# Kernel optimization log

Hardware: AMD Instinct MI355X
Metric: run time of the kernel (lower is better)

## Reference

```python
import jax, jax.numpy as jnp
import numpy as np

D_MODEL = 2048
N_HEADS = 16
HEAD_DIM = D_MODEL // N_HEADS


def setup_inputs() -> dict:
    key = jax.random.key(0)
    ks = jax.random.split(key, 9)
    s = 0.02
    B, S = 4, 2048
    return {
        "x": jax.random.normal(ks[0], (B, S, D_MODEL), dtype=jnp.float32),
        "Wq": jax.random.normal(ks[1], (D_MODEL, D_MODEL), dtype=jnp.float32) * s,
        "bq": jnp.zeros((D_MODEL,), dtype=jnp.float32),
        "Wk": jax.random.normal(ks[2], (D_MODEL, D_MODEL), dtype=jnp.float32) * s,
        "bk": jnp.zeros((D_MODEL,), dtype=jnp.float32),
        "Wv": jax.random.normal(ks[3], (D_MODEL, D_MODEL), dtype=jnp.float32) * s,
        "bv": jnp.zeros((D_MODEL,), dtype=jnp.float32),
        "Wo": jax.random.normal(ks[4], (D_MODEL, D_MODEL), dtype=jnp.float32) * s,
        "bo": jnp.zeros((D_MODEL,), dtype=jnp.float32),
    }


def reference(x, Wq, bq, Wk, bk, Wv, bv, Wo, bo):
    B, S, _ = x.shape
    scale = jnp.asarray(np.sqrt(HEAD_DIM), dtype=x.dtype)

    def split_heads(t):  # [B,S,D] -> [B,H,S,hd]
        return t.reshape(B, S, N_HEADS, HEAD_DIM).transpose(0, 2, 1, 3)

    q = split_heads(x @ Wq + bq)
    k = split_heads(x @ Wk + bk)
    v = split_heads(x @ Wv + bv)

    # scores: [B,H,S,S]
    attn = jnp.einsum('bhqd,bhkd->bhqk', q, k) / scale
    kv_len = S
    causal = jnp.triu(jnp.ones((S, kv_len), dtype=bool), k=kv_len - S + 1)
    attn = jnp.where(causal[None, None], -jnp.inf, attn)
    attn = jax.nn.softmax(attn, axis=-1)
    # dropout is identity (p=0 / eval mode)
    out = jnp.einsum('bhqk,bhkd->bhqd', attn, v)
    out = out.transpose(0, 2, 1, 3).reshape(B, S, D_MODEL)
    return out @ Wo + bo
```

## Files before the change

### kernel.cpp

```cpp
#include <hip/hip_runtime.h>
#include <hip/hip_bf16.h>

#define DEV __device__ __forceinline__

typedef __bf16 bf16_t;
typedef __bf16 bf16x8 __attribute__((ext_vector_type(8)));
typedef __bf16 bf16x4 __attribute__((ext_vector_type(4)));
typedef float f32x4 __attribute__((ext_vector_type(4)));
typedef float f32x16 __attribute__((ext_vector_type(16)));
typedef unsigned int u32;
typedef unsigned short u16;
typedef u32 u32x4 __attribute__((ext_vector_type(4)));

constexpr int D_MODEL = 2048;
constexpr int SEQ = 2048;
constexpr int BATCH = 4;
constexpr int N_HEADS = 16;
constexpr int HEAD_DIM = 128;
constexpr int TOK = BATCH * SEQ;

DEV void gload_lds16(const void* g, void* l) {
  __builtin_amdgcn_global_load_lds(
      (const __attribute__((address_space(1))) unsigned int*)g,
      (__attribute__((address_space(3))) unsigned int*)l, 16, 0, 0);
}

DEV float fast_exp2(float x) {
#if __has_builtin(__builtin_amdgcn_exp2f)
  return __builtin_amdgcn_exp2f(x);
#else
  return exp2f(x);
#endif
}

DEV u32 pack2(float lo, float hi) {
  u16 a = __builtin_bit_cast(u16, (bf16_t)lo);
  u16 b = __builtin_bit_cast(u16, (bf16_t)hi);
  return (u32)a | ((u32)b << 16);
}

#define MFMA16(a, b, c) __builtin_amdgcn_mfma_f32_16x16x32_bf16((a), (b), (c), 0, 0, 0)
#define MFMA32(a, b, c) __builtin_amdgcn_mfma_f32_32x32x16_bf16((a), (b), (c), 0, 0, 0)

__global__ void k_cvt(const float* __restrict__ in, bf16_t* __restrict__ out, int n4) {
  int i = blockIdx.x * blockDim.x + threadIdx.x;
  int stride = gridDim.x * blockDim.x;
  for (; i < n4; i += stride) {
    float4 v = ((const float4*)in)[i];
    bf16x4 o;
    o[0] = (bf16_t)v.x; o[1] = (bf16_t)v.y; o[2] = (bf16_t)v.z; o[3] = (bf16_t)v.w;
    ((bf16x4*)out)[i] = o;
  }
}

__global__ void k_transpose_w4(const float* __restrict__ Wq, const float* __restrict__ Wk,
                               const float* __restrict__ Wv, const float* __restrict__ Wo,
                               bf16_t* __restrict__ WqkvT, bf16_t* __restrict__ WoT) {
  __shared__ float t[32][33];
  const int z = blockIdx.z;
  const float* W = z == 0 ? Wq : z == 1 ? Wk : z == 2 ? Wv : Wo;
  bf16_t* Wt = z < 3 ? WqkvT + (size_t)z * D_MODEL * D_MODEL : WoT;
  int k0 = blockIdx.x * 32, n0 = blockIdx.y * 32;
  int tx = threadIdx.x, ty = threadIdx.y;
#pragma unroll
  for (int r = ty; r < 32; r += 8)
    t[r][tx] = W[(size_t)(k0 + r) * D_MODEL + n0 + tx];
  __syncthreads();
#pragma unroll
  for (int r = ty; r < 32; r += 8)
    Wt[(size_t)(n0 + r) * D_MODEL + k0 + tx] = (bf16_t)t[tx][r];
}

template <int MODE>
__global__ __launch_bounds__(512, 2) void k_gemm256(const bf16_t* __restrict__ A,
                                                    const bf16_t* __restrict__ Bt,
                                                    const float* __restrict__ b0p,
                                                    const float* __restrict__ b1p,
                                                    const float* __restrict__ b2p,
                                                    void* __restrict__ o0,
                                                    void* __restrict__ o1,
                                                    void* __restrict__ o2) {
  constexpr int K = D_MODEL;
  constexpr int NTOT = (MODE == 0) ? 3 * D_MODEL : D_MODEL;
  constexpr int NT = K / 64;
  __shared__ __attribute__((aligned(16))) bf16_t sh[2][2][2][8192];

  const int bid = blockIdx.x;
  const int nbn = NTOT / 256;
  const int cpx = gridDim.x >> 3;
  const int swz = (bid & 7) * cpx + (bid >> 3);
  const int bm = swz / nbn, bn = swz % nbn;

  const int tid = threadIdx.x;
  const int lane = tid & 63;
  const int w = tid >> 6;
  const int wm = w >> 2, wn = w & 3;
  const int lr = lane & 15, lg = lane >> 4;

  const bf16_t* Agl[2];
  const bf16_t* Bgl[2];
  int ldsg[2];
#pragma unroll
  for (int l = 0; l < 2; ++l) {
    int g = l * 512 + tid;
    int r = g >> 2, c = g & 3;
    int csw = c ^ ((r ^ (r >> 2)) & 3);
    Agl[l] = A + (size_t)(bm * 256 + r) * K + csw * 8;
    Bgl[l] = Bt + (size_t)(bn * 256 + r) * K + csw * 8;
    ldsg[l] = g * 8;
  }

  auto SA = [&](int buf, int t, int kh) {
    const int off = t * 64 + kh * 32;
#pragma unroll
    for (int l = 0; l < 2; ++l) gload_lds16(Agl[l] + off, &sh[buf][0][kh][ldsg[l]]);
  };
  auto SB = [&](int buf, int t, int kh) {
    const int off = t * 64 + kh * 32;
#pragma unroll
    for (int l = 0; l < 2; ++l) gload_lds16(Bgl[l] + off, &sh[buf][1][kh][ldsg[l]]);
  };

  int offA[8], offB[4];
  const int cx = lg ^ ((lr ^ (lr >> 2)) & 3);
#pragma unroll
  for (int i = 0; i < 8; ++i) offA[i] = (wm * 128 + i * 16 + lr) * 32 + cx * 8;
#pragma unroll
  for (int j = 0; j < 4; ++j) offB[j] = (wn * 64 + j * 16 + lr) * 32 + cx * 8;

  f32x4 acc[8][4] = {};
  bf16x8 a0[8], a1[8], bb[4];

  SA(0, 0, 0); SB(0, 0, 0); SA(0, 0, 1); SB(0, 0, 1); SA(1, 1, 0);

  for (int t = 0; t < NT; ++t) {
    const int cur = t & 1, nxt = cur ^ 1;
    const int t1 = (t + 1 < NT) ? t + 1 : NT - 1;
    const int t2 = (t + 2 < NT) ? t + 2 : NT - 1;

    asm volatile("s_waitcnt vmcnt(6)" ::: "memory");
    __builtin_amdgcn_s_barrier();
#pragma unroll
    for (int i = 0; i < 8; ++i) a0[i] = *(const bf16x8*)&sh[cur][0][0][offA[i]];
#pragma unroll
    for (int j = 0; j < 4; ++j) bb[j] = *(const bf16x8*)&sh[cur][1][0][offB[j]];
    SB(nxt, t1, 0);
    asm volatile("s_waitcnt lgkmcnt(0)" ::: "memory");
    __builtin_amdgcn_sched_barrier(0);
    __builtin_amdgcn_s_setprio(1);
#pragma unroll
    for (int i = 0; i < 8; ++i) {
      acc[i][0] = MFMA16(a0[i], bb[0], acc[i][0]);
      acc[i][1] = MFMA16(a0[i], bb[1], acc[i][1]);
    }
    __builtin_amdgcn_s_setprio(0);

    asm volatile("s_waitcnt vmcnt(6)" ::: "memory");
    __builtin_amdgcn_s_barrier();
#pragma unroll
    for (int i = 0; i < 8; ++i) a1[i] = *(const bf16x8*)&sh[cur][0][1][offA[i]];
    SA(nxt, t1, 1);
    asm volatile("s_waitcnt lgkmcnt(0)" ::: "memory");
    __builtin_amdgcn_sched_barrier(0);
    __builtin_amdgcn_s_setprio(1);
#pragma unroll
    for (int i = 0; i < 8; ++i) {
      acc[i][2] = MFMA16(a0[i], bb[2], acc[i][2]);
      acc[i][3] = MFMA16(a0[i], bb[3], acc[i][3]);
    }
    __builtin_amdgcn_s_setprio(0);

    asm volatile("s_waitcnt vmcnt(6)" ::: "memory");
    __builtin_amdgcn_s_barrier();
#pragma unroll
    for (int j = 0; j < 4; ++j) bb[j] = *(const bf16x8*)&sh[cur][1][1][offB[j]];
    SB(nxt, t1, 1);
    asm volatile("s_waitcnt lgkmcnt(0)" ::: "memory");
    __builtin_amdgcn_sched_barrier(0);
    __builtin_amdgcn_s_setprio(1);
#pragma unroll
    for (int i = 0; i < 8; ++i) {
      acc[i][0] = MFMA16(a1[i], bb[0], acc[i][0]);
      acc[i][1] = MFMA16(a1[i], bb[1], acc[i][1]);
    }
    __builtin_amdgcn_s_setprio(0);

    SA(cur, t2, 0);
    __builtin_amdgcn_s_setprio(1);
#pragma unroll
    for (int i = 0; i < 8; ++i) {
      acc[i][2] = MFMA16(a1[i], bb[2], acc[i][2]);
      acc[i][3] = MFMA16(a1[i], bb[3], acc[i][3]);
    }
    __builtin_amdgcn_s_setprio(0);
  }

#pragma unroll
  for (int i = 0; i < 8; ++i) {
    const int row = bm * 256 + wm * 128 + i * 16 + lg * 4;
#pragma unroll
    for (int jn = 0; jn < 4; ++jn) {
      const int col = bn * 256 + wn * 64 + jn * 16 + lr;
      if (MODE == 1) {
        const float bv = b0p[col];
        float* Cf = (float*)o0;
#pragma unroll
        for (int j = 0; j < 4; ++j)
          Cf[(size_t)(row + j) * D_MODEL + col] = acc[i][jn][j] + bv;
      } else {
        const int sel = col >> 11, cl = col & 2047;
        const float bv = (sel == 0 ? b0p : sel == 1 ? b1p : b2p)[cl];
        if (sel < 2) {
          bf16_t* dst = (bf16_t*)(sel == 0 ? o0 : o1);
#pragma unroll
          for (int j = 0; j < 4; ++j)
            dst[(size_t)(row + j) * D_MODEL + cl] = (bf16_t)(acc[i][jn][j] + bv);
        } else {
          const int bb2 = row >> 11, s = row & 2047;
          bf16x4 ov;
#pragma unroll
          for (int j = 0; j < 4; ++j) ov[j] = (bf16_t)(acc[i][jn][j] + bv);
          bf16_t* Vt = (bf16_t*)o2;
          *(bf16x4*)(Vt + (((size_t)(bb2 * 16 + (cl >> 7))) * 128 + (cl & 127)) * 2048 + s) = ov;
        }
      }
    }
  }
}

__global__ __launch_bounds__(256, 3) void k_attn(const bf16_t* __restrict__ Q,
                                                 const bf16_t* __restrict__ K,
                                                 const bf16_t* __restrict__ Vt,
                                                 bf16_t* __restrict__ AO) {
  const int fid = blockIdx.x;
  const int qb = 15 - (fid >> 6);
  const int bh = fid & 63;
  const int b = bh >> 4, h = bh & 15;
  const int w = threadIdx.x >> 6, lane = threadIdx.x & 63;
  const int l31 = lane & 31, hl = lane >> 5;
  const int nt = 4 * qb + 4;

  __shared__ __attribute__((aligned(16))) bf16_t Ks[2][32 * 128];
  __shared__ __attribute__((aligned(16))) bf16_t Vs[2][128 * 32];

  const bf16_t* kbase = K + (size_t)(b * SEQ) * D_MODEL + h * HEAD_DIM;
  const bf16_t* vtbase = Vt + (size_t)bh * HEAD_DIM * SEQ;
  const float C = 0.12751949848078418f;

  auto STAGE = [&](int buf, int kt) {
    const int tt = threadIdx.x;
#pragma unroll
    for (int p = 0; p < 2; ++p) {
      int g = p * 256 + tt;
      int r = g >> 4, c = g & 15;
      gload_lds16(kbase + (size_t)(kt * 32 + r) * D_MODEL + ((c ^ (r & 7)) * 8),
                  &Ks[buf][(size_t)(g & ~63) * 8]);
    }
#pragma unroll
    for (int p = 0; p < 2; ++p) {
      int g = p * 256 + tt;
      int r = g >> 2, c = g & 3;
      gload_lds16(vtbase + (size_t)r * SEQ + kt * 32 + ((c ^ ((r ^ (r >> 2)) & 3)) * 8),
                  &Vs[buf][(size_t)(g & ~63) * 8]);
    }
  };

  const int qw0 = qb * 128 + w * 32;
  const int qa = qw0 + l31;

  const bf16_t* qp = Q + (size_t)(b * SEQ + qa) * D_MODEL + h * HEAD_DIM + hl * 8;
  bf16x8 qf[8];
#pragma unroll
  for (int step = 0; step < 8; ++step) qf[step] = *(const bf16x8*)(qp + step * 16);

  f32x16 oacc[4];
#pragma unroll
  for (int db = 0; db < 4; ++db)
#pragma unroll
    for (int r = 0; r < 16; ++r) oacc[db][r] = 0.f;
  float m = -1e30f, lsum = 0.f;

  STAGE(0, 0);
  asm volatile("s_waitcnt vmcnt(0)" ::: "memory");
  __syncthreads();

  int buf = 0;
  for (int kt = 0; kt < nt; ++kt) {
    if (kt + 1 < nt) STAGE(buf ^ 1, kt + 1);

    if (kt * 32 < qw0 + 32) {
      f32x16 sacc;
#pragma unroll
      for (int r = 0; r < 16; ++r) sacc[r] = 0.f;
      const bf16_t* kr = &Ks[buf][l31 * 128];
      const int rx = l31 & 7;
      __builtin_amdgcn_s_setprio(1);
#pragma unroll
      for (int step = 0; step < 8; ++step) {
        bf16x8 kf = *(const bf16x8*)(kr + (((step * 2 + hl) ^ rx) * 8));
        sacc = MFMA32(kf, qf[step], sacc);
      }
      __builtin_amdgcn_s_setprio(0);

      const bool domask = (kt * 32 + 31 > qw0);
#pragma unroll
      for (int r = 0; r < 16; ++r) {
        float v = sacc[r] * C;
        if (domask) {
          int kv = kt * 32 + 4 * hl + (r & 3) + 8 * (r >> 2);
          if (kv > qa) v = -1e30f;
        }
        sacc[r] = v;
      }
      float mx8[8];
#pragma unroll
      for (int r = 0; r < 8; ++r) mx8[r] = fmaxf(sacc[r], sacc[r + 8]);
#pragma unroll
      for (int r = 0; r < 4; ++r) mx8[r] = fmaxf(mx8[r], mx8[r + 4]);
      float tm = fmaxf(fmaxf(mx8[0], mx8[1]), fmaxf(mx8[2], mx8[3]));
      tm = fmaxf(tm, __shfl_xor(tm, 32));

      if (!__all(tm <= m + 11.5f)) {
        const float mn = fmaxf(m, tm);
        const float al = fast_exp2(m - mn);
        lsum *= al;
#pragma unroll
        for (int db = 0; db < 4; ++db)
#pragma unroll
          for (int r = 0; r < 16; ++r) oacc[db][r] *= al;
        m = mn;
      }

#pragma unroll
      for (int r = 0; r < 16; ++r) sacc[r] = fast_exp2(sacc[r] - m);
      float sm8[8];
#pragma unroll
      for (int r = 0; r < 8; ++r) sm8[r] = sacc[r] + sacc[r + 8];
#pragma unroll
      for (int r = 0; r < 4; ++r) sm8[r] = sm8[r] + sm8[r + 4];
      float ls = (sm8[0] + sm8[1]) + (sm8[2] + sm8[3]);
      lsum += ls + __shfl_xor(ls, 32);

      bf16x8 pb[2];
#pragma unroll
      for (int ck = 0; ck < 2; ++ck) {
        u32 a0 = pack2(sacc[8 * ck + 0], sacc[8 * ck + 1]);
        u32 a1 = pack2(sacc[8 * ck + 2], sacc[8 * ck + 3]);
        u32 b0 = pack2(sacc[8 * ck + 4], sacc[8 * ck + 5]);
        u32 b1 = pack2(sacc[8 * ck + 6], sacc[8 * ck + 7]);
        u32 send0 = hl ? a0 : b0, send1 = hl ? a1 : b1;
        u32 keep0 = hl ? b0 : a0, keep1 = hl ? b1 : a1;
        u32 r0 = __shfl_xor(send0, 32), r1 = __shfl_xor(send1, 32);
        u32x4 fv;
        fv[0] = hl ? r0 : keep0;
        fv[1] = hl ? r1 : keep1;
        fv[2] = hl ? keep0 : r0;
        fv[3] = hl ? keep1 : r1;
        pb[ck] = __builtin_bit_cast(bf16x8, fv);
      }

      __builtin_amdgcn_s_setprio(1);
#pragma unroll
      for (int db = 0; db < 4; ++db) {
        const int vrow = db * 32 + l31;
        const bf16_t* vr = &Vs[buf][vrow * 32];
        const int vx = (vrow ^ (vrow >> 2)) & 3;
#pragma unroll
        for (int ck = 0; ck < 2; ++ck) {
          bf16x8 vf = *(const bf16x8*)(vr + (((ck * 2 + hl) ^ vx) * 8));
          oacc[db] = MFMA32(vf, pb[ck], oacc[db]);
        }
      }
      __builtin_amdgcn_s_setprio(0);
    }

    __syncthreads();
    buf ^= 1;
  }

  const float inv = 1.f / lsum;
  bf16_t* ao = AO + (size_t)(b * SEQ + qa) * D_MODEL + h * HEAD_DIM;
#pragma unroll
  for (int db = 0; db < 4; ++db)
#pragma unroll
    for (int g = 0; g < 4; ++g) {
      bf16x4 ov;
#pragma unroll
      for (int j = 0; j < 4; ++j) ov[j] = (bf16_t)(oacc[db][4 * g + j] * inv);
      *(bf16x4*)(ao + db * 32 + 8 * g + 4 * hl) = ov;
    }
}

extern "C" void kernel_launch(void* const* d_in, const int* in_sizes, int n_in,
                              void* d_out, int out_size, void* d_ws, size_t ws_size,
                              hipStream_t stream) {
  const float* x  = (const float*)d_in[0];
  const float* Wq = (const float*)d_in[1];
  const float* bq = (const float*)d_in[2];
  const float* Wk = (const float*)d_in[3];
  const float* bk = (const float*)d_in[4];
  const float* Wv = (const float*)d_in[5];
  const float* bv = (const float*)d_in[6];
  const float* Wo = (const float*)d_in[7];
  const float* bo = (const float*)d_in[8];

  const size_t SZ_X = (size_t)TOK * D_MODEL * sizeof(bf16_t);
  const size_t SZ_W = (size_t)D_MODEL * D_MODEL * sizeof(bf16_t);

  char* p = (char*)d_ws;
  bf16_t* xb    = (bf16_t*)p;                     p += SZ_X;
  bf16_t* WqkvT = (bf16_t*)p;                     p += 3 * SZ_W;
  bf16_t* WoT   = (bf16_t*)p;                     p += SZ_W;
  bf16_t* Qm    = (bf16_t*)p;                     p += SZ_X;
  bf16_t* Km    = (bf16_t*)p;                     p += SZ_X;
  bf16_t* Vt    = (bf16_t*)p;                     p += SZ_X;
  bf16_t* AO    = xb;

  k_cvt<<<2048, 256, 0, stream>>>(x, xb, TOK * D_MODEL / 4);

  dim3 tb(32, 8);
  k_transpose_w4<<<dim3(64, 64, 4), tb, 0, stream>>>(Wq, Wk, Wv, Wo, WqkvT, WoT);

  const int gqkv = (TOK / 256) * (3 * D_MODEL / 256);
  k_gemm256<0><<<gqkv, 512, 0, stream>>>(xb, WqkvT, bq, bk, bv, Qm, Km, Vt);

  k_attn<<<1024, 256, 0, stream>>>(Qm, Km, Vt, AO);

  const int go = (TOK / 256) * (D_MODEL / 256);
  k_gemm256<1><<<go, 512, 0, stream>>>(AO, WoT, bo, nullptr, nullptr, d_out, nullptr, nullptr);
}
```

Before: 422.4 us.

## Restructure GEMM main loop into per-k-half stages with staggered LDS waits

Replaces the four-phase software pipeline (separate a0/a1 fragment registers, three barriers, prefetch two tiles ahead) with a simpler two-phase loop over k-halves. Each phase loads B and A fragments from LDS, issues global→LDS prefetch for the next tile, then interleaves MFMA rows with partial lgkmcnt waits so compute starts before all LDS reads land. This cuts fragment register usage and the number of barriers per tile, but reduces prefetch depth from two tiles to one, which may expose global load latency.

```diff
diff --git a/kernel.cpp b/kernel.cpp
--- a/kernel.cpp
+++ b/kernel.cpp
@@ -129,71 +129,48 @@
   for (int j = 0; j < 4; ++j) offB[j] = (wn * 64 + j * 16 + lr) * 32 + cx * 8;
 
   f32x4 acc[8][4] = {};
-  bf16x8 a0[8], a1[8], bb[4];
-
-  SA(0, 0, 0); SB(0, 0, 0); SA(0, 0, 1); SB(0, 0, 1); SA(1, 1, 0);
+  bf16x8 af[8], bf_[4];
+
+  SA(0, 0, 0); SB(0, 0, 0); SA(0, 0, 1); SB(0, 0, 1);
+
+#define MFMA_ROW(i)                                  \
+  acc[i][0] = MFMA16(af[i], bf_[0], acc[i][0]);      \
+  acc[i][1] = MFMA16(af[i], bf_[1], acc[i][1]);      \
+  acc[i][2] = MFMA16(af[i], bf_[2], acc[i][2]);      \
+  acc[i][3] = MFMA16(af[i], bf_[3], acc[i][3]);
 
   for (int t = 0; t < NT; ++t) {
     const int cur = t & 1, nxt = cur ^ 1;
     const int t1 = (t + 1 < NT) ? t + 1 : NT - 1;
-    const int t2 = (t + 2 < NT) ? t + 2 : NT - 1;
-
-    asm volatile("s_waitcnt vmcnt(6)" ::: "memory");
-    __builtin_amdgcn_s_barrier();
-#pragma unroll
-    for (int i = 0; i < 8; ++i) a0[i] = *(const bf16x8*)&sh[cur][0][0][offA[i]];
-#pragma unroll
-    for (int j = 0; j < 4; ++j) bb[j] = *(const bf16x8*)&sh[cur][1][0][offB[j]];
-    SB(nxt, t1, 0);
-    asm volatile("s_waitcnt lgkmcnt(0)" ::: "memory");
-    __builtin_amdgcn_sched_barrier(0);
-    __builtin_amdgcn_s_setprio(1);
-#pragma unroll
-    for (int i = 0; i < 8; ++i) {
-      acc[i][0] = MFMA16(a0[i], bb[0], acc[i][0]);
-      acc[i][1] = MFMA16(a0[i], bb[1], acc[i][1]);
-    }
-    __builtin_amdgcn_s_setprio(0);
-
-    asm volatile("s_waitcnt vmcnt(6)" ::: "memory");
-    __builtin_amdgcn_s_barrier();
-#pragma unroll
-    for (int i = 0; i < 8; ++i) a1[i] = *(const bf16x8*)&sh[cur][0][1][offA[i]];
-    SA(nxt, t1, 1);
-    asm volatile("s_waitcnt lgkmcnt(0)" ::: "memory");
-    __builtin_amdgcn_sched_barrier(0);
-    __builtin_amdgcn_s_setprio(1);
-#pragma unroll
-    for (int i = 0; i < 8; ++i) {
-      acc[i][2] = MFMA16(a0[i], bb[2], acc[i][2]);
-      acc[i][3] = MFMA16(a0[i], bb[3], acc[i][3]);
-    }
-    __builtin_amdgcn_s_setprio(0);
-
-    asm volatile("s_waitcnt vmcnt(6)" ::: "memory");
-    __builtin_amdgcn_s_barrier();
-#pragma unroll
-    for (int j = 0; j < 4; ++j) bb[j] = *(const bf16x8*)&sh[cur][1][1][offB[j]];
-    SB(nxt, t1, 1);
-    asm volatile("s_waitcnt lgkmcnt(0)" ::: "memory");
-    __builtin_amdgcn_sched_barrier(0);
-    __builtin_amdgcn_s_setprio(1);
-#pragma unroll
-    for (int i = 0; i < 8; ++i) {
-      acc[i][0] = MFMA16(a1[i], bb[0], acc[i][0]);
-      acc[i][1] = MFMA16(a1[i], bb[1], acc[i][1]);
-    }
-    __builtin_amdgcn_s_setprio(0);
-
-    SA(cur, t2, 0);
-    __builtin_amdgcn_s_setprio(1);
-#pragma unroll
-    for (int i = 0; i < 8; ++i) {
-      acc[i][2] = MFMA16(a1[i], bb[2], acc[i][2]);
-      acc[i][3] = MFMA16(a1[i], bb[3], acc[i][3]);
-    }
-    __builtin_amdgcn_s_setprio(0);
+#pragma unroll
+    for (int kh = 0; kh < 2; ++kh) {
+      asm volatile("s_waitcnt vmcnt(4)" ::: "memory");
+      __builtin_amdgcn_s_barrier();
+#pragma unroll
+      for (int j = 0; j < 4; ++j) bf_[j] = *(const bf16x8*)&sh[cur][1][kh][offB[j]];
+#pragma unroll
+      for (int i = 0; i < 8; ++i) af[i] = *(const bf16x8*)&sh[cur][0][kh][offA[i]];
+      SA(nxt, t1, kh);
+      SB(nxt, t1, kh);
+      __builtin_amdgcn_s_setprio(1);
+      asm volatile("s_waitcnt lgkmcnt(6)" ::: "memory");
+      __builtin_amdgcn_sched_barrier(0);
+      MFMA_ROW(0) MFMA_ROW(1)
+      asm volatile("s_waitcnt lgkmcnt(4)" ::: "memory");
+      __builtin_amdgcn_sched_barrier(0);
+      MFMA_ROW(2) MFMA_ROW(3)
+      asm volatile("s_waitcnt lgkmcnt(2)" ::: "memory");
+      __builtin_amdgcn_sched_barrier(0);
+      MFMA_ROW(4) MFMA_ROW(5)
+      asm volatile("s_waitcnt lgkmcnt(0)" ::: "memory");
+      __builtin_amdgcn_sched_barrier(0);
+      MFMA_ROW(6) MFMA_ROW(7)
+      __builtin_amdgcn_s_setprio(0);
+    }
   }
+#undef MFMA_ROW
+
+  asm volatile("s_waitcnt vmcnt(0) lgkmcnt(0)" ::: "memory");
 
 #pragma unroll
   for (int i = 0; i < 8; ++i) {
```

Result: no change. 420.1 us (-0.5%).
